# Performance work log

Hardware: AMD Instinct MI355X
Metric: run time of the kernel (lower is better)

The kernel has to match this reference:

```python
import jax, jax.numpy as jnp
import numpy as np

N_NODES = 50000
N_EDGES = 800000
OBS_DIM = 25
HID = 128
EMB = 64
EDGE_DIM = 8
HEADS = 4
N_LAYERS = 3
COMM_RANGE = 1500.0
LN_EPS = 1e-5


def layernorm(x, g, b):
    mu = jnp.mean(x, axis=-1, keepdims=True)
    var = jnp.mean((x - mu) ** 2, axis=-1, keepdims=True)
    return (x - mu) / jnp.sqrt(var + LN_EPS) * g + b


def setup_inputs() -> dict:
    key = jax.random.key(0)
    ks = iter(jax.random.split(key, 64))

    def w(shape, s=0.05):
        return (jax.random.normal(next(ks), shape, jnp.float32) * s).astype(jnp.float32)

    inp = {}
    inp["observations"] = jax.random.normal(next(ks), (N_NODES, OBS_DIM), jnp.float32)
    inp["positions"] = jax.random.uniform(next(ks), (N_NODES, 2), jnp.float32) * 1000.0
    inp["edge_index"] = jax.random.randint(next(ks), (2, N_EDGES), 0, N_NODES, jnp.int32)
    # node encoder (obs_encoder branch: Linear-LN-ReLU-Linear-ReLU)
    inp["enc_w1"] = w((OBS_DIM, HID)); inp["enc_b1"] = w((HID,), 0.01)
    inp["enc_ln_g"] = jnp.ones((HID,), jnp.float32); inp["enc_ln_b"] = jnp.zeros((HID,), jnp.float32)
    inp["enc_w2"] = w((HID, EMB)); inp["enc_b2"] = w((EMB,), 0.01)
    cat_dim = 2 * EMB + EDGE_DIM  # 136
    # per-layer GNN params, stacked over layers
    inp["msg_w1"] = w((N_LAYERS, cat_dim, HID)); inp["msg_b1"] = w((N_LAYERS, HID), 0.01)
    inp["msg_w2"] = w((N_LAYERS, HID, EMB)); inp["msg_b2"] = w((N_LAYERS, EMB), 0.01)
    inp["att_w1"] = w((N_LAYERS, cat_dim, HID)); inp["att_b1"] = w((N_LAYERS, HID), 0.01)
    inp["att_w2"] = w((N_LAYERS, HID, HEADS)); inp["att_b2"] = w((N_LAYERS, HEADS), 0.01)
    inp["upd_w1"] = w((N_LAYERS, 2 * EMB, HID)); inp["upd_b1"] = w((N_LAYERS, HID), 0.01)
    inp["upd_w2"] = w((N_LAYERS, HID, EMB)); inp["upd_b2"] = w((N_LAYERS, EMB), 0.01)
    inp["ln_g"] = jnp.ones((N_LAYERS, EMB), jnp.float32); inp["ln_b"] = jnp.zeros((N_LAYERS, EMB), jnp.float32)
    # output projection
    inp["out_w1"] = w((EMB, HID)); inp["out_b1"] = w((HID,), 0.01)
    inp["out_w2"] = w((HID, EMB)); inp["out_b2"] = w((EMB,), 0.01)
    return inp


def reference(observations, positions, edge_index,
              enc_w1, enc_b1, enc_ln_g, enc_ln_b, enc_w2, enc_b2,
              msg_w1, msg_b1, msg_w2, msg_b2,
              att_w1, att_b1, att_w2, att_b2,
              upd_w1, upd_b1, upd_w2, upd_b2,
              ln_g, ln_b,
              out_w1, out_b1, out_w2, out_b2):
    n = observations.shape[0]
    # --- node encoder (use_full_obs=True path) ---
    h = observations @ enc_w1 + enc_b1
    h = jax.nn.relu(layernorm(h, enc_ln_g, enc_ln_b))
    x = jax.nn.relu(h @ enc_w2 + enc_b2)  # [N, EMB]

    # --- edge features (build_graph math, edges given) ---
    src, dst = edge_index[0], edge_index[1]
    rel = positions[dst] - positions[src]                    # [E, 2]
    dist = jnp.linalg.norm(rel, axis=-1, keepdims=True)      # [E, 1]
    rel_n = rel / (dist + 1e-6)
    dist_n = dist / COMM_RANGE
    angle = jnp.arctan2(rel[:, 1], rel[:, 0])[:, None]
    edge_attr = jnp.concatenate(
        [dist_n, rel_n, jnp.cos(angle), jnp.sin(angle), dist_n ** 2,
         jnp.zeros((rel.shape[0], 2), x.dtype)], axis=-1)    # [E, 8]

    # --- GNN communication layers (PyG: x_i = target = dst, x_j = source = src,
    #     aggregate to dst; dropout inactive at inference) ---
    for l in range(N_LAYERS):
        cat = jnp.concatenate([x[dst], x[src], edge_attr], axis=-1)       # [E, 136]
        m = jax.nn.relu(cat @ msg_w1[l] + msg_b1[l]) @ msg_w2[l] + msg_b2[l]   # [E, EMB]
        a = jax.nn.relu(cat @ att_w1[l] + att_b1[l]) @ att_w2[l] + att_b2[l]   # [E, HEADS]
        wgt = jnp.mean(jax.nn.softmax(a, axis=-1), axis=-1, keepdims=True)     # [E, 1]
        aggr = jax.ops.segment_sum(m * wgt, dst, num_segments=n)               # [N, EMB]
        upd_in = jnp.concatenate([x, aggr], axis=-1)                            # [N, 2*EMB]
        upd = jax.nn.relu(upd_in @ upd_w1[l] + upd_b1[l]) @ upd_w2[l] + upd_b2[l]
        x = layernorm(x + upd, ln_g[l], ln_b[l])

    # --- output projection ---
    return jax.nn.relu(x @ out_w1 + out_b1) @ out_w2 + out_b2
```

## Files before the change

kernel.cpp:

```cpp
#include <hip/hip_runtime.h>
#include <hip/hip_bf16.h>

typedef unsigned short ushort_t;
typedef unsigned int uint_t;

constexpr int OBS  = 25;
constexpr int HID  = 128;
constexpr int EMB  = 64;
constexpr int CAT  = 136;
constexpr int NN   = 50000;

constexpr int TE      = 128;
constexpr int ETHR    = 512;
constexpr int K1PAD   = 148;
constexpr int K2PAD   = 140;
constexpr int K1STEPS = 9;
constexpr int K2STEPS = 8;

constexpr int TB = 128;

typedef __attribute__((ext_vector_type(8)))  short bf16x8;
typedef __attribute__((ext_vector_type(16))) float f32x16;
typedef __attribute__((ext_vector_type(4)))  uint_t uint4v;

__device__ __forceinline__ ushort_t f2bf(float f) {
    union { float f; uint_t u; } v; v.f = f;
    uint_t r = v.u + 0x7FFFu + ((v.u >> 16) & 1u);
    return (ushort_t)(r >> 16);
}

__device__ __forceinline__ bf16x8 ld8(const ushort_t* p) {
    uint2 lo = *reinterpret_cast<const uint2*>(p);
    uint2 hi = *reinterpret_cast<const uint2*>(p + 4);
    uint4 u = make_uint4(lo.x, lo.y, hi.x, hi.y);
// ... 50 lines not shown
    int e = blockIdx.x * 256 + threadIdx.x;
    if (e >= ne) return;
    int s = src[e], d = dst[e];
    float rx = pos[d * 2 + 0] - pos[s * 2 + 0];
    float ry = pos[d * 2 + 1] - pos[s * 2 + 1];
    float dist = sqrtf(rx * rx + ry * ry);
    float inv = 1.f / (dist + 1e-6f);
    float dn = dist * (1.f / 1500.f);
    uint_t ux = (uint_t)f2bf(dn) | ((uint_t)f2bf(rx * inv) << 16);
    uint_t uy = (uint_t)f2bf(ry * inv) | ((dist > 0.f ? 0u : 1u) << 16);
    int p = atomicAdd(&ofs[d], 1);
    uint4v ev = { ux, uy, (uint_t)s, (uint_t)d };
    eab4[p] = ev;
}

__global__ __launch_bounds__(256) void k_prep(
    const float* __restrict__ w1, const float* __restrict__ w2,
    ushort_t* __restrict__ w1t, ushort_t* __restrict__ w2t)
{
    int t = blockIdx.x * 256 + threadIdx.x;
    const int n1 = 3 * HID * K1PAD;
    if (t < n1) {
        int l = t / (HID * K1PAD), rem = t % (HID * K1PAD);
        int c = rem / K1PAD, k = rem % K1PAD;
        float v = (k < CAT) ? w1[(size_t)l * CAT * HID + (size_t)k * HID + c] : 0.f;
        w1t[t] = f2bf(v);
    }
    const int n2 = 3 * EMB * K2PAD;
    if (t < n2) {
        int l = t / (EMB * K2PAD), rem = t % (EMB * K2PAD);
        int c = rem / K2PAD, k = rem % K2PAD;
        float v = (k < HID) ? w2[(size_t)l * HID * EMB + (size_t)k * EMB + c] : 0.f;
        w2t[t] = f2bf(v);
    }
}

constexpr int EKP = 36;
__global__ __launch_bounds__(256, 1) void k_encoder_mfma(
    const float* __restrict__ obs,
    const float* __restrict__ w1, const float* __restrict__ b1,
    const float* __restrict__ lng, const float* __restrict__ lnb,
    const float* __restrict__ w2, const float* __restrict__ b2,
    float* __restrict__ x, ushort_t* __restrict__ xb, int n)
{
    __shared__ __align__(16) ushort_t s_OB[TB * EKP];
    __shared__ __align__(16) ushort_t s_B1[HID * EKP];
    __shared__ __align__(16) float    s_G[TB * 132];
    __shared__ __align__(16) ushort_t s_H[TB * K2PAD];
    __shared__ __align__(16) ushort_t s_W2[EMB * K2PAD];

    const int tid = threadIdx.x;
    const int lane = tid & 63, wid = tid >> 6;
    const int wr = wid >> 1, wc = wid & 1;
    const int l31 = lane & 31, lhi = lane >> 5;
    const int n0 = blockIdx.x * TB;

    for (int i = tid; i < TB * 32; i += 256) {
        int row = i >> 5, k = i & 31;
        int gn = n0 + row;
        float v = (gn < n && k < OBS) ? obs[(size_t)gn * OBS + k] : 0.f;
        s_OB[row * EKP + k] = f2bf(v);
    }
    for (int i = tid; i < 32 * HID; i += 256) {
        int k = i >> 7, c = i & 127;
        float v = (k < OBS) ? w1[k * HID + c] : 0.f;
        s_B1[c * EKP + k] = f2bf(v);
    }
    __syncthreads();

    f32x16 a00, a01, a10, a11;
    {
        float bv0 = b1[wc * 64 + l31], bv1 = b1[wc * 64 + 32 + l31];
#pragma unroll
        for (int i = 0; i < 16; ++i) { a00[i] = bv0; a01[i] = bv1; a10[i] = bv0; a11[i] = bv1; }
    }
    {
        const ushort_t* aR0 = s_OB + (wr * 64 + l31) * EKP;
        const ushort_t* aR1 = aR0 + 32 * EKP;
        const ushort_t* bR0 = s_B1 + (wc * 64 + l31) * EKP;
        const ushort_t* bR1 = bR0 + 32 * EKP;
        const int koff = lhi * 8;
#pragma unroll
        for (int s = 0; s < 2; ++s) {
            const int ke = s * 16 + koff;
            bf16x8 av0 = ld8(aR0 + ke), av1 = ld8(aR1 + ke);
            bf16x8 bv0 = ld8(bR0 + ke), bv1 = ld8(bR1 + ke);
            a00 = __builtin_amdgcn_mfma_f32_32x32x16_bf16(av0, bv0, a00, 0, 0, 0);
            a01 = __builtin_amdgcn_mfma_f32_32x32x16_bf16(av0, bv1, a01, 0, 0, 0);
            a10 = __builtin_amdgcn_mfma_f32_32x32x16_bf16(av1, bv0, a10, 0, 0, 0);
            a11 = __builtin_amdgcn_mfma_f32_32x32x16_bf16(av1, bv1, a11, 0, 0, 0);
        }
    }
#define WRITE_G(ACC, SUB, NC)                                                  \
    {                                                                          \
        const int col = wc * 64 + (NC) * 32 + l31;                             \
        _Pragma("unroll")                                                      \
        for (int r = 0; r < 16; ++r) {                                         \
            int row = wr * 64 + (SUB) * 32 + CROW(r, lhi);                     \
            s_G[row * 132 + col] = ACC[r];                                     \
        }                                                                      \
    }
    WRITE_G(a00, 0, 0) WRITE_G(a01, 0, 1) WRITE_G(a10, 1, 0) WRITE_G(a11, 1, 1)
#undef WRITE_G
    __syncthreads();

    for (int i = tid; i < HID * EMB; i += 256) {
        int k = i >> 6, c = i & 63;
        s_W2[c * K2PAD + k] = f2bf(w2[i]);
    }
    if (tid < TB) {
        float sum = 0.f, sum2 = 0.f;
        const float* gr = s_G + tid * 132;
#pragma unroll 8
        for (int q = 0; q < HID; ++q) { float v = gr[q]; sum += v; sum2 += v * v; }
        float mu = sum * (1.f / HID);
        float var = fmaxf(sum2 * (1.f / HID) - mu * mu, 0.f);
        float rs = 1.f / sqrtf(var + 1e-5f);
        ushort_t* hr = s_H + tid * K2PAD;
#pragma unroll 8
        for (int q = 0; q < HID; ++q) {
            float v = (gr[q] - mu) * rs * lng[q] + lnb[q];
            hr[q] = f2bf(fmaxf(v, 0.f));
        }
    }
    __syncthreads();

    f32x16 c0, c1;
    {
        float bv = b2[wc * 32 + l31];
#pragma unroll
        for (int i = 0; i < 16; ++i) { c0[i] = bv; c1[i] = bv; }
    }
    {
        const ushort_t* aR0 = s_H + (wr * 64 + l31) * K2PAD;
        const ushort_t* aR1 = aR0 + 32 * K2PAD;
        const ushort_t* bR = s_W2 + (wc * 32 + l31) * K2PAD;
        const int koff = lhi * 8;
#pragma unroll
        for (int s = 0; s < K2STEPS; ++s) {
            const int ke = s * 16 + koff;
            bf16x8 av0 = ld8(aR0 + ke), av1 = ld8(aR1 + ke);
            bf16x8 bv = ld8(bR + ke);
            c0 = __builtin_amdgcn_mfma_f32_32x32x16_bf16(av0, bv, c0, 0, 0, 0);
            c1 = __builtin_amdgcn_mfma_f32_32x32x16_bf16(av1, bv, c1, 0, 0, 0);
        }
    }
    {
        const int col = wc * 32 + l31;
#define STORE_X(CC, SUB)                                                       \
        {                                                                      \
            _Pragma("unroll")                                                  \
            for (int r = 0; r < 16; ++r) {                                     \
                int row = wr * 64 + (SUB) * 32 + CROW(r, lhi);                 \
                int gn = n0 + row;                                             \
                if (gn < n) {                                                  \
                    float v = fmaxf(CC[r], 0.f);                               \
                    x[(size_t)gn * EMB + col] = v;                             \
                    xb[(size_t)gn * EMB + col] = f2bf(v);                      \
                }                                                              \
            }                                                                  \
        }
        STORE_X(c0, 0) STORE_X(c1, 1)
#undef STORE_X
    }
}

__global__ __launch_bounds__(ETHR, 8) void k_edge_mfma(
    const ushort_t* __restrict__ xb,
    const uint4v* __restrict__ eab4,
    const ushort_t* __restrict__ w1t,
    const float* __restrict__ b1,
    const ushort_t* __restrict__ w2t,
    const float* __restrict__ b2,
    float* __restrict__ aggr, int ne)
{
    __shared__ __align__(16) ushort_t s_A[TE * K1PAD];
    __shared__ int s_dst[TE];
    ushort_t* s_H = s_A;
// ... 57 lines not shown
        const ushort_t* bR0 = w1t + (wc * 64 + l31) * K1PAD;
        const ushort_t* bR1 = bR0 + 32 * K1PAD;
        const int koff = lhi * 8;
#pragma unroll
        for (int s = 0; s < K1STEPS; ++s) {
            const int ke = s * 16 + koff;
            bf16x8 av = ld8(aR + ke);
            bf16x8 bv0 = ld8(bR0 + ke);
            bf16x8 bv1 = ld8(bR1 + ke);
            a0 = __builtin_amdgcn_mfma_f32_32x32x16_bf16(av, bv0, a0, 0, 0, 0);
            a1 = __builtin_amdgcn_mfma_f32_32x32x16_bf16(av, bv1, a1, 0, 0, 0);
        }
    }
    __syncthreads();

#define WRITE_H(ACC, NC)                                                       \
    {                                                                          \
        const int col = wc * 64 + (NC) * 32 + l31;                             \
        _Pragma("unroll")                                                      \
        for (int r = 0; r < 16; ++r) {                                         \
            int row = wr * 32 + CROW(r, lhi);                                  \
            s_H[row * K2PAD + col] = f2bf(fmaxf(ACC[r], 0.f));                 \
        }                                                                      \
    }
    WRITE_H(a0, 0) WRITE_H(a1, 1)
#undef WRITE_H
    __syncthreads();

    f32x16 c0;
    {
        float bv = b2[wc * 32 + l31];
#pragma unroll
        for (int i = 0; i < 16; ++i) c0[i] = bv;
    }
    {
        const ushort_t* aR = s_H + (wr * 32 + l31) * K2PAD;
        const ushort_t* bR = w2t + (wc * 32 + l31) * K2PAD;
        const int koff = lhi * 8;
#pragma unroll
        for (int s = 0; s < K2STEPS; ++s) {
            const int ke = s * 16 + koff;
// ... 20 lines not shown
        float acc = 0.f;
#pragma unroll 8
        for (int r = 0; r < 32; ++r) {
            int d = s_dst[base + r];
            float v = s_M[(base + r) * 68 + col];
            if (d != cur) {
                atomicAdd(aggr + (size_t)cur * EMB + col, acc);
                acc = 0.f; cur = d;
            }
            acc += v;
        }
        atomicAdd(aggr + (size_t)cur * EMB + col, acc);
    }
}

__global__ __launch_bounds__(256, 2) void k_update_mfma(
    float* __restrict__ x, ushort_t* __restrict__ xb,
    float* __restrict__ aggr,
    const float* __restrict__ w1, const float* __restrict__ b1,
    const float* __restrict__ w2, const float* __restrict__ b2,
    const float* __restrict__ g, const float* __restrict__ bb, int n)
{
    __shared__ __align__(16) ushort_t s_A[TB * K2PAD];
    __shared__ __align__(16) ushort_t s_B[TB * K2PAD];
    ushort_t* s_H  = s_A;
    ushort_t* s_W2 = s_B;
    float*    s_U  = reinterpret_cast<float*>(s_B);

    const int tid = threadIdx.x;
    const int lane = tid & 63, wid = tid >> 6;
    const int wr = wid >> 1, wc = wid & 1;
    const int l31 = lane & 31, lhi = lane >> 5;
    const int n0 = blockIdx.x * TB;

    {
        const int row = tid >> 1, h = tid & 1;
        const int gn = n0 + row;
        ushort_t* arow = s_A + row * K2PAD;
        if (h == 0) {
            uint2* dp = reinterpret_cast<uint2*>(arow);
            if (gn < n) {
                const uint2* sp = reinterpret_cast<const uint2*>(xb + (size_t)gn * EMB);
#pragma unroll
                for (int i = 0; i < 16; ++i) dp[i] = sp[i];
            } else {
                const uint2 z = make_uint2(0u, 0u);
#pragma unroll
                for (int i = 0; i < 16; ++i) dp[i] = z;
            }
        } else {
            if (gn < n) {
                float4* sp = reinterpret_cast<float4*>(aggr + (size_t)gn * EMB);
                const float4 z4 = make_float4(0.f, 0.f, 0.f, 0.f);
#pragma unroll
                for (int i = 0; i < 16; ++i) {
                    float4 v = sp[i];
                    sp[i] = z4;
                    ushort_t* qq = arow + EMB + i * 4;
                    qq[0] = f2bf(v.x); qq[1] = f2bf(v.y); qq[2] = f2bf(v.z); qq[3] = f2bf(v.w);
                }
            } else {
#pragma unroll
                for (int i = 0; i < 16; ++i) {
                    ushort_t* qq = arow + EMB + i * 4;
                    qq[0] = 0; qq[1] = 0; qq[2] = 0; qq[3] = 0;
                }
            }
        }
    }
    for (int i = tid; i < 128 * 128; i += 256) {
        int k = i >> 7, c = i & 127;
        s_B[c * K2PAD + k] = f2bf(w1[i]);
    }
    __syncthreads();

    f32x16 a00, a01, a10, a11;
    {
        float bv0 = b1[wc * 64 + l31], bv1 = b1[wc * 64 + 32 + l31];
#pragma unroll
        for (int i = 0; i < 16; ++i) { a00[i] = bv0; a01[i] = bv1; a10[i] = bv0; a11[i] = bv1; }
    }
    {
        const ushort_t* aR0 = s_A + (wr * 64 + l31) * K2PAD;
        const ushort_t* aR1 = aR0 + 32 * K2PAD;
        const ushort_t* bR0 = s_B + (wc * 64 + l31) * K2PAD;
        const ushort_t* bR1 = bR0 + 32 * K2PAD;
        const int koff = lhi * 8;
#pragma unroll
        for (int s = 0; s < K2STEPS; ++s) {
            const int ke = s * 16 + koff;
            bf16x8 av0 = ld8(aR0 + ke), av1 = ld8(aR1 + ke);
            bf16x8 bv0 = ld8(bR0 + ke), bv1 = ld8(bR1 + ke);
            a00 = __builtin_amdgcn_mfma_f32_32x32x16_bf16(av0, bv0, a00, 0, 0, 0);
            a01 = __builtin_amdgcn_mfma_f32_32x32x16_bf16(av0, bv1, a01, 0, 0, 0);
            a10 = __builtin_amdgcn_mfma_f32_32x32x16_bf16(av1, bv0, a10, 0, 0, 0);
            a11 = __builtin_amdgcn_mfma_f32_32x32x16_bf16(av1, bv1, a11, 0, 0, 0);
        }
    }
    __syncthreads();

#define WRITE_H(ACC, SUB, NC)                                                  \
    {                                                                          \
        const int col = wc * 64 + (NC) * 32 + l31;                             \
        _Pragma("unroll")                                                      \
        for (int r = 0; r < 16; ++r) {                                         \
            int row = wr * 64 + (SUB) * 32 + CROW(r, lhi);                     \
            s_H[row * K2PAD + col] = f2bf(fmaxf(ACC[r], 0.f));                 \
        }                                                                      \
    }
    WRITE_H(a00, 0, 0) WRITE_H(a01, 0, 1) WRITE_H(a10, 1, 0) WRITE_H(a11, 1, 1)
#undef WRITE_H
    for (int i = tid; i < HID * EMB; i += 256) {
        int k = i >> 6, c = i & 63;
        s_W2[c * K2PAD + k] = f2bf(w2[i]);
    }
    __syncthreads();

    f32x16 c0, c1;
    {
        float bv = b2[wc * 32 + l31];
#pragma unroll
        for (int i = 0; i < 16; ++i) { c0[i] = bv; c1[i] = bv; }
    }
    {
        const ushort_t* aR0 = s_H + (wr * 64 + l31) * K2PAD;
        const ushort_t* aR1 = aR0 + 32 * K2PAD;
        const ushort_t* bR = s_W2 + (wc * 32 + l31) * K2PAD;
        const int koff = lhi * 8;
#pragma unroll
        for (int s = 0; s < K2STEPS; ++s) {
            const int ke = s * 16 + koff;
            bf16x8 av0 = ld8(aR0 + ke), av1 = ld8(aR1 + ke);
            bf16x8 bv = ld8(bR + ke);
            c0 = __builtin_amdgcn_mfma_f32_32x32x16_bf16(av0, bv, c0, 0, 0, 0);
            c1 = __builtin_amdgcn_mfma_f32_32x32x16_bf16(av1, bv, c1, 0, 0, 0);
        }
    }
    __syncthreads();

    {
        const int col = wc * 32 + l31;
#pragma unroll
        for (int r = 0; r < 16; ++r) {
            int row = wr * 64 + CROW(r, lhi);
            s_U[row * 68 + col] = c0[r];
            s_U[(row + 32) * 68 + col] = c1[r];
        }
    }
    __syncthreads();

    if (tid < TB) {
        int gn = n0 + tid;
        if (gn < n) {
            const float* xr = x + (size_t)gn * EMB;
            float* ur = s_U + tid * 68;
            float sum = 0.f, sum2 = 0.f;
#pragma unroll 8
            for (int q = 0; q < EMB; ++q) {
                float v = xr[q] + ur[q];
                ur[q] = v;
                sum += v; sum2 += v * v;
            }
            float mu = sum * (1.f / EMB);
            float var = fmaxf(sum2 * (1.f / EMB) - mu * mu, 0.f);
            float rs = 1.f / sqrtf(var + 1e-5f);
            float* xo = x + (size_t)gn * EMB;
            ushort_t* xbo = xb + (size_t)gn * EMB;
#pragma unroll 8
            for (int q = 0; q < EMB; ++q) {
                float v = (ur[q] - mu) * rs * g[q] + bb[q];
                xo[q] = v;
                xbo[q] = f2bf(v);
            }
        }
    }
}

constexpr int OKP = 68;
__global__ __launch_bounds__(256, 2) void k_output_mfma(
    const ushort_t* __restrict__ xb,
    const float* __restrict__ w1, const float* __restrict__ b1,
    const float* __restrict__ w2, const float* __restrict__ b2,
    float* __restrict__ out, int n)
{
    __shared__ __align__(16) ushort_t s_A[TB * OKP];
    __shared__ __align__(16) ushort_t s_B[HID * OKP];
    __shared__ __align__(16) ushort_t s_H[TB * K2PAD];
    __shared__ __align__(16) ushort_t s_W2[EMB * K2PAD];

    const int tid = threadIdx.x;
    const int lane = tid & 63, wid = tid >> 6;
    const int wr = wid >> 1, wc = wid & 1;
    const int l31 = lane & 31, lhi = lane >> 5;
    const int n0 = blockIdx.x * TB;

    for (int i = tid; i < TB * 16; i += 256) {
        int row = i >> 4, q = i & 15;
        int gn = n0 + row;
        uint2 v = make_uint2(0u, 0u);
        if (gn < n) v = reinterpret_cast<const uint2*>(xb + (size_t)gn * EMB)[q];
        *reinterpret_cast<uint2*>(s_A + row * OKP + q * 4) = v;
    }
    for (int i = tid; i < EMB * HID; i += 256) {
        int k = i >> 7, c = i & 127;
        s_B[c * OKP + k] = f2bf(w1[i]);
    }
    for (int i = tid; i < HID * EMB; i += 256) {
        int k = i >> 6, c = i & 63;
        s_W2[c * K2PAD + k] = f2bf(w2[i]);
    }
    __syncthreads();

    f32x16 a00, a01, a10, a11;
    {
        float bv0 = b1[wc * 64 + l31], bv1 = b1[wc * 64 + 32 + l31];
#pragma unroll
        for (int i = 0; i < 16; ++i) { a00[i] = bv0; a01[i] = bv1; a10[i] = bv0; a11[i] = bv1; }
    }
    {
        const ushort_t* aR0 = s_A + (wr * 64 + l31) * OKP;
        const ushort_t* aR1 = aR0 + 32 * OKP;
        const ushort_t* bR0 = s_B + (wc * 64 + l31) * OKP;
        const ushort_t* bR1 = bR0 + 32 * OKP;
        const int koff = lhi * 8;
#pragma unroll
        for (int s = 0; s < 4; ++s) {
            const int ke = s * 16 + koff;
            bf16x8 av0 = ld8(aR0 + ke), av1 = ld8(aR1 + ke);
            bf16x8 bv0 = ld8(bR0 + ke), bv1 = ld8(bR1 + ke);
            a00 = __builtin_amdgcn_mfma_f32_32x32x16_bf16(av0, bv0, a00, 0, 0, 0);
            a01 = __builtin_amdgcn_mfma_f32_32x32x16_bf16(av0, bv1, a01, 0, 0, 0);
            a10 = __builtin_amdgcn_mfma_f32_32x32x16_bf16(av1, bv0, a10, 0, 0, 0);
            a11 = __builtin_amdgcn_mfma_f32_32x32x16_bf16(av1, bv1, a11, 0, 0, 0);
        }
    }
    __syncthreads();

#define WRITE_H(ACC, SUB, NC)                                                  \
    {                                                                          \
        const int col = wc * 64 + (NC) * 32 + l31;                             \
        _Pragma("unroll")                                                      \
        for (int r = 0; r < 16; ++r) {                                         \
            int row = wr * 64 + (SUB) * 32 + CROW(r, lhi);                     \
            s_H[row * K2PAD + col] = f2bf(fmaxf(ACC[r], 0.f));                 \
        }                                                                      \
    }
    WRITE_H(a00, 0, 0) WRITE_H(a01, 0, 1) WRITE_H(a10, 1, 0) WRITE_H(a11, 1, 1)
#undef WRITE_H
    __syncthreads();

    f32x16 c0, c1;
    {
        float bv = b2[wc * 32 + l31];
#pragma unroll
        for (int i = 0; i < 16; ++i) { c0[i] = bv; c1[i] = bv; }
    }
    {
        const ushort_t* aR0 = s_H + (wr * 64 + l31) * K2PAD;
        const ushort_t* aR1 = aR0 + 32 * K2PAD;
        const ushort_t* bR = s_W2 + (wc * 32 + l31) * K2PAD;
        const int koff = lhi * 8;
#pragma unroll
        for (int s = 0; s < K2STEPS; ++s) {
            const int ke = s * 16 + koff;
            bf16x8 av0 = ld8(aR0 + ke), av1 = ld8(aR1 + ke);
            bf16x8 bv = ld8(bR + ke);
            c0 = __builtin_amdgcn_mfma_f32_32x32x16_bf16(av0, bv, c0, 0, 0, 0);
            c1 = __builtin_amdgcn_mfma_f32_32x32x16_bf16(av1, bv, c1, 0, 0, 0);
        }
    }
    {
        const int col = wc * 32 + l31;
#pragma unroll
        for (int r = 0; r < 16; ++r) {
            int row0 = wr * 64 + CROW(r, lhi);
            int g0 = n0 + row0, g1 = g0 + 32;
            if (g0 < n) out[(size_t)g0 * EMB + col] = c0[r];
            if (g1 < n) out[(size_t)g1 * EMB + col] = c1[r];
        }
    }
}

extern "C" void kernel_launch(void* const* d_in, const int* in_sizes, int n_in,
                              void* d_out, int out_size, void* d_ws, size_t ws_size,
                              hipStream_t stream)
{
    const float* obs     = (const float*)d_in[0];
    const float* pos     = (const float*)d_in[1];
    const int*   eidx    = (const int*)d_in[2];
    const float* enc_w1  = (const float*)d_in[3];
    const float* enc_b1  = (const float*)d_in[4];
    const float* enc_lng = (const float*)d_in[5];
    const float* enc_lnb = (const float*)d_in[6];
// ... 12 lines not shown
    const float* out_w1  = (const float*)d_in[23];
    const float* out_b1  = (const float*)d_in[24];
    const float* out_w2  = (const float*)d_in[25];
    const float* out_b2  = (const float*)d_in[26];

    const int n  = in_sizes[0] / OBS;
    const int ne = in_sizes[2] / 2;
    const int* src = eidx;
    const int* dst = eidx + ne;

    char* ws = (char*)d_ws;
    float*    x     = (float*)ws;
    ushort_t* xbuf  = (ushort_t*)(ws + 12800000);
    uint4v*   eab4  = (uint4v*)(ws + 19200000);
    float*    aggr  = (float*)(ws + 32000000);
    ushort_t* w1t   = (ushort_t*)(ws + 44800000);
    ushort_t* w2t   = (ushort_t*)(ws + 44913664);
    int*      hist  = (int*)(ws + 44967424);
    int*      scan  = (int*)(ws + 45167424);
    int*      bsum  = (int*)(ws + 45367424);

    const int NB1 = (NN + 511) / 512;
    const int nb  = (n + TB - 1) / TB;

    hipMemsetAsync(hist, 0, NN * sizeof(int), stream);
    k_hist<<<(ne + 255) / 256, 256, 0, stream>>>(dst, hist, ne);
    k_scan1<<<NB1, 512, 0, stream>>>(hist, scan, bsum, NN);
    k_scan3<<<NB1, 512, 0, stream>>>(scan, bsum, NN);
    k_scatter_feat<<<(ne + 255) / 256, 256, 0, stream>>>(pos, src, dst, scan,
                                                         eab4, ne);

    k_prep<<<(3 * HID * K1PAD + 255) / 256, 256, 0, stream>>>(msg_w1, msg_w2, w1t, w2t);
    k_encoder_mfma<<<nb, 256, 0, stream>>>(obs, enc_w1, enc_b1, enc_lng, enc_lnb,
                                           enc_w2, enc_b2, x, xbuf, n);
    hipMemsetAsync(aggr, 0, (size_t)n * EMB * sizeof(float), stream);

    for (int l = 0; l < 3; ++l) {
        k_edge_mfma<<<ne / TE, ETHR, 0, stream>>>(
            xbuf, eab4,
            w1t + (size_t)l * HID * K1PAD, msg_b1 + (size_t)l * HID,
            w2t + (size_t)l * EMB * K2PAD, msg_b2 + (size_t)l * EMB,
            aggr, ne);
        k_update_mfma<<<nb, 256, 0, stream>>>(
            x, xbuf, aggr,
            upd_w1 + (size_t)l * 2 * EMB * HID, upd_b1 + (size_t)l * HID,
            upd_w2 + (size_t)l * HID * EMB, upd_b2 + (size_t)l * EMB,
            ln_g + (size_t)l * EMB, ln_b + (size_t)l * EMB, n);
    }
    k_output_mfma<<<nb, 256, 0, stream>>>(
        xbuf, out_w1, out_b1, out_w2, out_b2, (float*)d_out, n);
}
```

Before: 713.8 us.

## Pretranspose all weights once, shrink node tiles, fuse output projection into last update

Every weight matrix (update, encoder, output) is now converted to padded transposed bf16 in one prep kernel, so node kernels read MFMA B-operands straight from global memory instead of rebuilding them in shared memory per block. Node kernels use 64-row tiles with less LDS, allowing higher occupancy (launch bounds raised to 2 and 4 blocks per CU). The output MLP is fused into the final update kernel through a flag, which removes one launch and one pass over the node features. In exchange, B-operand reads now go through cache rather than LDS, and the extra prep work adds some overhead.

After: 678.3 us. -5.0%, faster.

```diff
diff --git a/kernel.cpp b/kernel.cpp
--- a/kernel.cpp
+++ b/kernel.cpp
@@ -17,7 +17,9 @@
 constexpr int K1STEPS = 9;
 constexpr int K2STEPS = 8;
 
-constexpr int TB = 128;
+constexpr int TBN = 64;
+constexpr int EKP = 36;
+constexpr int XKP = 68;
 
 typedef __attribute__((ext_vector_type(8)))  short bf16x8;
 typedef __attribute__((ext_vector_type(16))) float f32x16;
@@ -98,101 +100,118 @@
     eab4[p] = ev;
 }
 
-__global__ __launch_bounds__(256) void k_prep(
-    const float* __restrict__ w1, const float* __restrict__ w2,
-    ushort_t* __restrict__ w1t, ushort_t* __restrict__ w2t)
+__global__ __launch_bounds__(256) void k_prep_all(
+    const float* __restrict__ msg_w1, const float* __restrict__ msg_w2,
+    const float* __restrict__ upd_w1, const float* __restrict__ upd_w2,
+    const float* __restrict__ enc_w1, const float* __restrict__ enc_w2,
+    const float* __restrict__ out_w1, const float* __restrict__ out_w2,
+    ushort_t* __restrict__ mw1t, ushort_t* __restrict__ mw2t,
+    ushort_t* __restrict__ uw1t, ushort_t* __restrict__ uw2t,
+    ushort_t* __restrict__ ew1t, ushort_t* __restrict__ ew2t,
+    ushort_t* __restrict__ ow1t, ushort_t* __restrict__ ow2t)
 {
     int t = blockIdx.x * 256 + threadIdx.x;
-    const int n1 = 3 * HID * K1PAD;
-    if (t < n1) {
-        int l = t / (HID * K1PAD), rem = t % (HID * K1PAD);
-        int c = rem / K1PAD, k = rem % K1PAD;
-        float v = (k < CAT) ? w1[(size_t)l * CAT * HID + (size_t)k * HID + c] : 0.f;
-        w1t[t] = f2bf(v);
-    }
-    const int n2 = 3 * EMB * K2PAD;
-    if (t < n2) {
-        int l = t / (EMB * K2PAD), rem = t % (EMB * K2PAD);
-        int c = rem / K2PAD, k = rem % K2PAD;
-        float v = (k < HID) ? w2[(size_t)l * HID * EMB + (size_t)k * EMB + c] : 0.f;
-        w2t[t] = f2bf(v);
-    }
-}
-
-constexpr int EKP = 36;
-__global__ __launch_bounds__(256, 1) void k_encoder_mfma(
+    const int S0 = 3 * HID * K1PAD, S1 = 3 * EMB * K2PAD;
+    const int S2 = 3 * HID * K2PAD, S3 = 3 * EMB * K2PAD;
+    const int S4 = HID * EKP, S5 = EMB * K2PAD;
+    const int S6 = HID * XKP, S7 = EMB * K2PAD;
+    if (t < S0) {
+        int l = t / (HID * K1PAD), r = t % (HID * K1PAD), c = r / K1PAD, k = r % K1PAD;
+        mw1t[t] = f2bf(k < CAT ? msg_w1[(size_t)l * CAT * HID + (size_t)k * HID + c] : 0.f);
+        return;
+    } t -= S0;
+    if (t < S1) {
+        int l = t / (EMB * K2PAD), r = t % (EMB * K2PAD), c = r / K2PAD, k = r % K2PAD;
+        mw2t[t] = f2bf(k < HID ? msg_w2[(size_t)l * HID * EMB + (size_t)k * EMB + c] : 0.f);
+        return;
+    } t -= S1;
+    if (t < S2) {
+        int l = t / (HID * K2PAD), r = t % (HID * K2PAD), c = r / K2PAD, k = r % K2PAD;
+        uw1t[t] = f2bf(k < 2 * EMB ? upd_w1[(size_t)l * 2 * EMB * HID + (size_t)k * HID + c] : 0.f);
+        return;
+    } t -= S2;
+    if (t < S3) {
+        int l = t / (EMB * K2PAD), r = t % (EMB * K2PAD), c = r / K2PAD, k = r % K2PAD;
+        uw2t[t] = f2bf(k < HID ? upd_w2[(size_t)l * HID * EMB + (size_t)k * EMB + c] : 0.f);
+        return;
+    } t -= S3;
+    if (t < S4) {
+        int c = t / EKP, k = t % EKP;
+        ew1t[t] = f2bf(k < OBS ? enc_w1[(size_t)k * HID + c] : 0.f);
+        return;
+    } t -= S4;
+    if (t < S5) {
+        int c = t / K2PAD, k = t % K2PAD;
+        ew2t[t] = f2bf(k < HID ? enc_w2[(size_t)k * EMB + c] : 0.f);
+        return;
+    } t -= S5;
+    if (t < S6) {
+        int c = t / XKP, k = t % XKP;
+        ow1t[t] = f2bf(k < EMB ? out_w1[(size_t)k * HID + c] : 0.f);
+        return;
+    } t -= S6;
+    if (t < S7) {
+        int c = t / K2PAD, k = t % K2PAD;
+        ow2t[t] = f2bf(k < HID ? out_w2[(size_t)k * EMB + c] : 0.f);
+    }
+}
+
+__global__ __launch_bounds__(256, 2) void k_encoder_mfma(
     const float* __restrict__ obs,
-    const float* __restrict__ w1, const float* __restrict__ b1,
+    const ushort_t* __restrict__ w1t, const float* __restrict__ b1,
     const float* __restrict__ lng, const float* __restrict__ lnb,
-    const float* __restrict__ w2, const float* __restrict__ b2,
+    const ushort_t* __restrict__ w2t, const float* __restrict__ b2,
     float* __restrict__ x, ushort_t* __restrict__ xb, int n)
 {
-    __shared__ __align__(16) ushort_t s_OB[TB * EKP];
-    __shared__ __align__(16) ushort_t s_B1[HID * EKP];
-    __shared__ __align__(16) float    s_G[TB * 132];
-    __shared__ __align__(16) ushort_t s_H[TB * K2PAD];
-    __shared__ __align__(16) ushort_t s_W2[EMB * K2PAD];
+    __shared__ __align__(16) ushort_t s_OB[TBN * EKP];
+    __shared__ __align__(16) float    s_G[TBN * 132];
+    __shared__ __align__(16) ushort_t s_H[TBN * K2PAD];
 
     const int tid = threadIdx.x;
     const int lane = tid & 63, wid = tid >> 6;
-    const int wr = wid >> 1, wc = wid & 1;
+    const int wr = wid >> 1, wc2 = wid & 1;
+    const int wr2 = wid & 1, wc3 = wid >> 1;
     const int l31 = lane & 31, lhi = lane >> 5;
-    const int n0 = blockIdx.x * TB;
-
-    for (int i = tid; i < TB * 32; i += 256) {
+    const int n0 = blockIdx.x * TBN;
+
+    for (int i = tid; i < TBN * 32; i += 256) {
         int row = i >> 5, k = i & 31;
         int gn = n0 + row;
-        float v = (gn < n && k < OBS) ? obs[(size_t)gn * OBS + k] : 0.f;
-        s_OB[row * EKP + k] = f2bf(v);
-    }
-    for (int i = tid; i < 32 * HID; i += 256) {
-        int k = i >> 7, c = i & 127;
-        float v = (k < OBS) ? w1[k * HID + c] : 0.f;
-        s_B1[c * EKP + k] = f2bf(v);
-    }
-    __syncthreads();
-
-    f32x16 a00, a01, a10, a11;
-    {
-        float bv0 = b1[wc * 64 + l31], bv1 = b1[wc * 64 + 32 + l31];
-#pragma unroll
-        for (int i = 0; i < 16; ++i) { a00[i] = bv0; a01[i] = bv1; a10[i] = bv0; a11[i] = bv1; }
-    }
-    {
-        const ushort_t* aR0 = s_OB + (wr * 64 + l31) * EKP;
-        const ushort_t* aR1 = aR0 + 32 * EKP;
-        const ushort_t* bR0 = s_B1 + (wc * 64 + l31) * EKP;
+        s_OB[row * EKP + k] = f2bf((gn < n && k < OBS) ? obs[(size_t)gn * OBS + k] : 0.f);
+    }
+    __syncthreads();
+
+    f32x16 a0, a1;
+    {
+        float bv0 = b1[wc2 * 64 + l31], bv1 = b1[wc2 * 64 + 32 + l31];
+#pragma unroll
+        for (int i = 0; i < 16; ++i) { a0[i] = bv0; a1[i] = bv1; }
+    }
+    {
+        const ushort_t* aR = s_OB + (wr * 32 + l31) * EKP;
+        const ushort_t* bR0 = w1t + (wc2 * 64 + l31) * EKP;
         const ushort_t* bR1 = bR0 + 32 * EKP;
         const int koff = lhi * 8;
 #pragma unroll
         for (int s = 0; s < 2; ++s) {
             const int ke = s * 16 + koff;
-            bf16x8 av0 = ld8(aR0 + ke), av1 = ld8(aR1 + ke);
+            bf16x8 av = ld8(aR + ke);
             bf16x8 bv0 = ld8(bR0 + ke), bv1 = ld8(bR1 + ke);
-            a00 = __builtin_amdgcn_mfma_f32_32x32x16_bf16(av0, bv0, a00, 0, 0, 0);
-            a01 = __builtin_amdgcn_mfma_f32_32x32x16_bf16(av0, bv1, a01, 0, 0, 0);
-            a10 = __builtin_amdgcn_mfma_f32_32x32x16_bf16(av1, bv0, a10, 0, 0, 0);
-            a11 = __builtin_amdgcn_mfma_f32_32x32x16_bf16(av1, bv1, a11, 0, 0, 0);
-        }
-    }
-#define WRITE_G(ACC, SUB, NC)                                                  \
-    {                                                                          \
-        const int col = wc * 64 + (NC) * 32 + l31;                             \
-        _Pragma("unroll")                                                      \
-        for (int r = 0; r < 16; ++r) {                                         \
-            int row = wr * 64 + (SUB) * 32 + CROW(r, lhi);                     \
-            s_G[row * 132 + col] = ACC[r];                                     \
-        }                                                                      \
-    }
-    WRITE_G(a00, 0, 0) WRITE_G(a01, 0, 1) WRITE_G(a10, 1, 0) WRITE_G(a11, 1, 1)
-#undef WRITE_G
-    __syncthreads();
-
-    for (int i = tid; i < HID * EMB; i += 256) {
-        int k = i >> 6, c = i & 63;
-        s_W2[c * K2PAD + k] = f2bf(w2[i]);
-    }
-    if (tid < TB) {
+            a0 = __builtin_amdgcn_mfma_f32_32x32x16_bf16(av, bv0, a0, 0, 0, 0);
+            a1 = __builtin_amdgcn_mfma_f32_32x32x16_bf16(av, bv1, a1, 0, 0, 0);
+        }
+    }
+    {
+#pragma unroll
+        for (int r = 0; r < 16; ++r) {
+            int row = wr * 32 + CROW(r, lhi);
+            s_G[row * 132 + wc2 * 64 + l31] = a0[r];
+            s_G[row * 132 + wc2 * 64 + 32 + l31] = a1[r];
+        }
+    }
+    __syncthreads();
+
+    if (tid < TBN) {
         float sum = 0.f, sum2 = 0.f;
         const float* gr = s_G + tid * 132;
 #pragma unroll 8
@@ -209,43 +228,35 @@
     }
     __syncthreads();
 
-    f32x16 c0, c1;
-    {
-        float bv = b2[wc * 32 + l31];
-#pragma unroll
-        for (int i = 0; i < 16; ++i) { c0[i] = bv; c1[i] = bv; }
-    }
-    {
-        const ushort_t* aR0 = s_H + (wr * 64 + l31) * K2PAD;
-        const ushort_t* aR1 = aR0 + 32 * K2PAD;
-        const ushort_t* bR = s_W2 + (wc * 32 + l31) * K2PAD;
+    f32x16 c0;
+    {
+        float bv = b2[wc3 * 32 + l31];
+#pragma unroll
+        for (int i = 0; i < 16; ++i) c0[i] = bv;
+    }
+    {
+        const ushort_t* aR = s_H + (wr2 * 32 + l31) * K2PAD;
+        const ushort_t* bR = w2t + (wc3 * 32 + l31) * K2PAD;
         const int koff = lhi * 8;
 #pragma unroll
         for (int s = 0; s < K2STEPS; ++s) {
             const int ke = s * 16 + koff;
-            bf16x8 av0 = ld8(aR0 + ke), av1 = ld8(aR1 + ke);
+            bf16x8 av = ld8(aR + ke);
             bf16x8 bv = ld8(bR + ke);
-            c0 = __builtin_amdgcn_mfma_f32_32x32x16_bf16(av0, bv, c0, 0, 0, 0);
-            c1 = __builtin_amdgcn_mfma_f32_32x32x16_bf16(av1, bv, c1, 0, 0, 0);
-        }
-    }
-    {
-        const int col = wc * 32 + l31;
-#define STORE_X(CC, SUB)                                                       \
-        {                                                                      \
-            _Pragma("unroll")                                                  \
-            for (int r = 0; r < 16; ++r) {                                     \
-                int row = wr * 64 + (SUB) * 32 + CROW(r, lhi);                 \
-                int gn = n0 + row;                                             \
-                if (gn < n) {                                                  \
-                    float v = fmaxf(CC[r], 0.f);                               \
-                    x[(size_t)gn * EMB + col] = v;                             \
-                    xb[(size_t)gn * EMB + col] = f2bf(v);                      \
-                }                                                              \
-            }                                                                  \
-        }
-        STORE_X(c0, 0) STORE_X(c1, 1)
-#undef STORE_X
+            c0 = __builtin_amdgcn_mfma_f32_32x32x16_bf16(av, bv, c0, 0, 0, 0);
+        }
+    }
+    {
+        const int col = wc3 * 32 + l31;
+#pragma unroll
+        for (int r = 0; r < 16; ++r) {
+            int g = n0 + wr2 * 32 + CROW(r, lhi);
+            if (g < n) {
+                float v = fmaxf(c0[r], 0.f);
+                x[(size_t)g * EMB + col] = v;
+                xb[(size_t)g * EMB + col] = f2bf(v);
+            }
+        }
     }
 }
 
@@ -333,7 +344,7 @@
     }
     __syncthreads();
 
-#define WRITE_H(ACC, NC)                                                       \
+#define WRITE_HE(ACC, NC)                                                      \
     {                                                                          \
         const int col = wc * 64 + (NC) * 32 + l31;                             \
         _Pragma("unroll")                                                      \
@@ -342,8 +353,8 @@
             s_H[row * K2PAD + col] = f2bf(fmaxf(ACC[r], 0.f));                 \
         }                                                                      \
     }
-    WRITE_H(a0, 0) WRITE_H(a1, 1)
-#undef WRITE_H
+    WRITE_HE(a0, 0) WRITE_HE(a1, 1)
+#undef WRITE_HE
     __syncthreads();
 
     f32x16 c0;
@@ -394,269 +405,230 @@
     }
 }
 
-__global__ __launch_bounds__(256, 2) void k_update_mfma(
+__global__ __launch_bounds__(256, 4) void k_update_mfma(
     float* __restrict__ x, ushort_t* __restrict__ xb,
     float* __restrict__ aggr,
-    const float* __restrict__ w1, const float* __restrict__ b1,
-    const float* __restrict__ w2, const float* __restrict__ b2,
-    const float* __restrict__ g, const float* __restrict__ bb, int n)
-{
-    __shared__ __align__(16) ushort_t s_A[TB * K2PAD];
-    __shared__ __align__(16) ushort_t s_B[TB * K2PAD];
-    ushort_t* s_H  = s_A;
-    ushort_t* s_W2 = s_B;
-    float*    s_U  = reinterpret_cast<float*>(s_B);
+    const ushort_t* __restrict__ w1t, const float* __restrict__ b1,
+    const ushort_t* __restrict__ w2t, const float* __restrict__ b2,
+    const float* __restrict__ g, const float* __restrict__ bb,
+    const ushort_t* __restrict__ ow1t, const float* __restrict__ ob1,
+    const ushort_t* __restrict__ ow2t, const float* __restrict__ ob2,
+    float* __restrict__ out, int fuse, int n)
+{
+    __shared__ __align__(16) ushort_t s_big[TBN * K2PAD];
+    __shared__ __align__(16) ushort_t s_Xn[TBN * XKP];
+    ushort_t* s_A = s_big;
+    ushort_t* s_H = s_big;
+    float*    s_U = reinterpret_cast<float*>(s_big);
 
     const int tid = threadIdx.x;
     const int lane = tid & 63, wid = tid >> 6;
-    const int wr = wid >> 1, wc = wid & 1;
+    const int wr = wid >> 1, wc2 = wid & 1;
+    const int wr2 = wid & 1, wc3 = wid >> 1;
     const int l31 = lane & 31, lhi = lane >> 5;
-    const int n0 = blockIdx.x * TB;
-
-    {
-        const int row = tid >> 1, h = tid & 1;
+    const int n0 = blockIdx.x * TBN;
+
+    {
+        const int row = tid >> 2, h = tid & 3;
         const int gn = n0 + row;
         ushort_t* arow = s_A + row * K2PAD;
-        if (h == 0) {
-            uint2* dp = reinterpret_cast<uint2*>(arow);
+        if (h < 2) {
+            uint2* dp = reinterpret_cast<uint2*>(arow) + h * 8;
             if (gn < n) {
-                const uint2* sp = reinterpret_cast<const uint2*>(xb + (size_t)gn * EMB);
-#pragma unroll
-                for (int i = 0; i < 16; ++i) dp[i] = sp[i];
+                const uint2* sp = reinterpret_cast<const uint2*>(xb + (size_t)gn * EMB) + h * 8;
+#pragma unroll
+                for (int i = 0; i < 8; ++i) dp[i] = sp[i];
             } else {
                 const uint2 z = make_uint2(0u, 0u);
 #pragma unroll
-                for (int i = 0; i < 16; ++i) dp[i] = z;
+                for (int i = 0; i < 8; ++i) dp[i] = z;
             }
         } else {
+            const int hh = h - 2;
+            uint_t* dp32 = reinterpret_cast<uint_t*>(arow + EMB + hh * 32);
             if (gn < n) {
-                float4* sp = reinterpret_cast<float4*>(aggr + (size_t)gn * EMB);
+                float4* sp = reinterpret_cast<float4*>(aggr + (size_t)gn * EMB + hh * 32);
                 const float4 z4 = make_float4(0.f, 0.f, 0.f, 0.f);
 #pragma unroll
-                for (int i = 0; i < 16; ++i) {
+                for (int i = 0; i < 8; ++i) {
                     float4 v = sp[i];
                     sp[i] = z4;
-                    ushort_t* qq = arow + EMB + i * 4;
-                    qq[0] = f2bf(v.x); qq[1] = f2bf(v.y); qq[2] = f2bf(v.z); qq[3] = f2bf(v.w);
+                    dp32[2 * i]     = (uint_t)f2bf(v.x) | ((uint_t)f2bf(v.y) << 16);
+                    dp32[2 * i + 1] = (uint_t)f2bf(v.z) | ((uint_t)f2bf(v.w) << 16);
                 }
             } else {
 #pragma unroll
-                for (int i = 0; i < 16; ++i) {
-                    ushort_t* qq = arow + EMB + i * 4;
-                    qq[0] = 0; qq[1] = 0; qq[2] = 0; qq[3] = 0;
+                for (int i = 0; i < 16; ++i) dp32[i] = 0u;
+            }
+        }
+    }
+    __syncthreads();
+
+    f32x16 a0, a1;
+    {
+        float bv0 = b1[wc2 * 64 + l31], bv1 = b1[wc2 * 64 + 32 + l31];
+#pragma unroll
+        for (int i = 0; i < 16; ++i) { a0[i] = bv0; a1[i] = bv1; }
+    }
+    {
+        const ushort_t* aR = s_A + (wr * 32 + l31) * K2PAD;
+        const ushort_t* bR0 = w1t + (wc2 * 64 + l31) * K2PAD;
+        const ushort_t* bR1 = bR0 + 32 * K2PAD;
+        const int koff = lhi * 8;
+#pragma unroll
+        for (int s = 0; s < K2STEPS; ++s) {
+            const int ke = s * 16 + koff;
+            bf16x8 av = ld8(aR + ke);
+            bf16x8 bv0 = ld8(bR0 + ke), bv1 = ld8(bR1 + ke);
+            a0 = __builtin_amdgcn_mfma_f32_32x32x16_bf16(av, bv0, a0, 0, 0, 0);
+            a1 = __builtin_amdgcn_mfma_f32_32x32x16_bf16(av, bv1, a1, 0, 0, 0);
+        }
+    }
+    __syncthreads();
+
+#define WRITE_HU(ACC, NC)                                                      \
+    {                                                                          \
+        const int col = wc2 * 64 + (NC) * 32 + l31;                            \
+        _Pragma("unroll")                                                      \
+        for (int r = 0; r < 16; ++r) {                                         \
+            int row = wr * 32 + CROW(r, lhi);                                  \
+            s_H[row * K2PAD + col] = f2bf(fmaxf(ACC[r], 0.f));                 \
+        }                                                                      \
+    }
+    WRITE_HU(a0, 0) WRITE_HU(a1, 1)
+    __syncthreads();
+
+    f32x16 c0;
+    {
+        float bv = b2[wc3 * 32 + l31];
+#pragma unroll
+        for (int i = 0; i < 16; ++i) c0[i] = bv;
+    }
+    {
+        const ushort_t* aR = s_H + (wr2 * 32 + l31) * K2PAD;
+        const ushort_t* bR = w2t + (wc3 * 32 + l31) * K2PAD;
+        const int koff = lhi * 8;
+#pragma unroll
+        for (int s = 0; s < K2STEPS; ++s) {
+            const int ke = s * 16 + koff;
+            bf16x8 av = ld8(aR + ke);
+            bf16x8 bv = ld8(bR + ke);
+            c0 = __builtin_amdgcn_mfma_f32_32x32x16_bf16(av, bv, c0, 0, 0, 0);
+        }
+    }
+    __syncthreads();
+
+    {
+        const int col = wc3 * 32 + l31;
+#pragma unroll
+        for (int r = 0; r < 16; ++r) {
+            int row = wr2 * 32 + CROW(r, lhi);
+            s_U[row * 68 + col] = c0[r];
+        }
+    }
+    __syncthreads();
+
+    if (!fuse) {
+        if (tid < TBN) {
+            int gn = n0 + tid;
+            if (gn < n) {
+                const float* xr = x + (size_t)gn * EMB;
+                float* ur = s_U + tid * 68;
+                float sum = 0.f, sum2 = 0.f;
+#pragma unroll 8
+                for (int q = 0; q < EMB; ++q) {
+                    float v = xr[q] + ur[q];
+                    ur[q] = v;
+                    sum += v; sum2 += v * v;
+                }
+                float mu = sum * (1.f / EMB);
+                float var = fmaxf(sum2 * (1.f / EMB) - mu * mu, 0.f);
+                float rs = 1.f / sqrtf(var + 1e-5f);
+                float* xo = x + (size_t)gn * EMB;
+                ushort_t* xbo = xb + (size_t)gn * EMB;
+#pragma unroll 8
+                for (int q = 0; q < EMB; ++q) {
+                    float v = (ur[q] - mu) * rs * g[q] + bb[q];
+                    xo[q] = v;
+                    xbo[q] = f2bf(v);
                 }
             }
         }
-    }
-    for (int i = tid; i < 128 * 128; i += 256) {
-        int k = i >> 7, c = i & 127;
-        s_B[c * K2PAD + k] = f2bf(w1[i]);
-    }
-    __syncthreads();
-
-    f32x16 a00, a01, a10, a11;
-    {
-        float bv0 = b1[wc * 64 + l31], bv1 = b1[wc * 64 + 32 + l31];
-#pragma unroll
-        for (int i = 0; i < 16; ++i) { a00[i] = bv0; a01[i] = bv1; a10[i] = bv0; a11[i] = bv1; }
-    }
-    {
-        const ushort_t* aR0 = s_A + (wr * 64 + l31) * K2PAD;
-        const ushort_t* aR1 = aR0 + 32 * K2PAD;
-        const ushort_t* bR0 = s_B + (wc * 64 + l31) * K2PAD;
-        const ushort_t* bR1 = bR0 + 32 * K2PAD;
-        const int koff = lhi * 8;
-#pragma unroll
-        for (int s = 0; s < K2STEPS; ++s) {
-            const int ke = s * 16 + koff;
-            bf16x8 av0 = ld8(aR0 + ke), av1 = ld8(aR1 + ke);
-            bf16x8 bv0 = ld8(bR0 + ke), bv1 = ld8(bR1 + ke);
-            a00 = __builtin_amdgcn_mfma_f32_32x32x16_bf16(av0, bv0, a00, 0, 0, 0);
-            a01 = __builtin_amdgcn_mfma_f32_32x32x16_bf16(av0, bv1, a01, 0, 0, 0);
-            a10 = __builtin_amdgcn_mfma_f32_32x32x16_bf16(av1, bv0, a10, 0, 0, 0);
-            a11 = __builtin_amdgcn_mfma_f32_32x32x16_bf16(av1, bv1, a11, 0, 0, 0);
-        }
-    }
-    __syncthreads();
-
-#define WRITE_H(ACC, SUB, NC)                                                  \
-    {                                                                          \
-        const int col = wc * 64 + (NC) * 32 + l31;                             \
-        _Pragma("unroll")                                                      \
-        for (int r = 0; r < 16; ++r) {                                         \
-            int row = wr * 64 + (SUB) * 32 + CROW(r, lhi);                     \
-            s_H[row * K2PAD + col] = f2bf(fmaxf(ACC[r], 0.f));                 \
-        }                                                                      \
-    }
-    WRITE_H(a00, 0, 0) WRITE_H(a01, 0, 1) WRITE_H(a10, 1, 0) WRITE_H(a11, 1, 1)
-#undef WRITE_H
-    for (int i = tid; i < HID * EMB; i += 256) {
-        int k = i >> 6, c = i & 63;
-        s_W2[c * K2PAD + k] = f2bf(w2[i]);
-    }
-    __syncthreads();
-
-    f32x16 c0, c1;
-    {
-        float bv = b2[wc * 32 + l31];
-#pragma unroll
-        for (int i = 0; i < 16; ++i) { c0[i] = bv; c1[i] = bv; }
-    }
-    {
-        const ushort_t* aR0 = s_H + (wr * 64 + l31) * K2PAD;
-        const ushort_t* aR1 = aR0 + 32 * K2PAD;
-        const ushort_t* bR = s_W2 + (wc * 32 + l31) * K2PAD;
-        const int koff = lhi * 8;
-#pragma unroll
-        for (int s = 0; s < K2STEPS; ++s) {
-            const int ke = s * 16 + koff;
-            bf16x8 av0 = ld8(aR0 + ke), av1 = ld8(aR1 + ke);
-            bf16x8 bv = ld8(bR + ke);
-            c0 = __builtin_amdgcn_mfma_f32_32x32x16_bf16(av0, bv, c0, 0, 0, 0);
-            c1 = __builtin_amdgcn_mfma_f32_32x32x16_bf16(av1, bv, c1, 0, 0, 0);
-        }
-    }
-    __syncthreads();
-
-    {
-        const int col = wc * 32 + l31;
-#pragma unroll
-        for (int r = 0; r < 16; ++r) {
-            int row = wr * 64 + CROW(r, lhi);
-            s_U[row * 68 + col] = c0[r];
-            s_U[(row + 32) * 68 + col] = c1[r];
-        }
-    }
-    __syncthreads();
-
-    if (tid < TB) {
+        return;
+    }
+
+    if (tid < TBN) {
         int gn = n0 + tid;
         if (gn < n) {
             const float* xr = x + (size_t)gn * EMB;
-            float* ur = s_U + tid * 68;
+            const float* ur = s_U + tid * 68;
             float sum = 0.f, sum2 = 0.f;
 #pragma unroll 8
             for (int q = 0; q < EMB; ++q) {
                 float v = xr[q] + ur[q];
-                ur[q] = v;
                 sum += v; sum2 += v * v;
             }
             float mu = sum * (1.f / EMB);
             float var = fmaxf(sum2 * (1.f / EMB) - mu * mu, 0.f);
             float rs = 1.f / sqrtf(var + 1e-5f);
-            float* xo = x + (size_t)gn * EMB;
-            ushort_t* xbo = xb + (size_t)gn * EMB;
+            ushort_t* xnr = s_Xn + tid * XKP;
 #pragma unroll 8
             for (int q = 0; q < EMB; ++q) {
-                float v = (ur[q] - mu) * rs * g[q] + bb[q];
-                xo[q] = v;
-                xbo[q] = f2bf(v);
+                float v = (xr[q] + ur[q] - mu) * rs * g[q] + bb[q];
+                xnr[q] = f2bf(v);
             }
         }
     }
-}
-
-constexpr int OKP = 68;
-__global__ __launch_bounds__(256, 2) void k_output_mfma(
-    const ushort_t* __restrict__ xb,
-    const float* __restrict__ w1, const float* __restrict__ b1,
-    const float* __restrict__ w2, const float* __restrict__ b2,
-    float* __restrict__ out, int n)
-{
-    __shared__ __align__(16) ushort_t s_A[TB * OKP];
-    __shared__ __align__(16) ushort_t s_B[HID * OKP];
-    __shared__ __align__(16) ushort_t s_H[TB * K2PAD];
-    __shared__ __align__(16) ushort_t s_W2[EMB * K2PAD];
-
-    const int tid = threadIdx.x;
-    const int lane = tid & 63, wid = tid >> 6;
-    const int wr = wid >> 1, wc = wid & 1;
-    const int l31 = lane & 31, lhi = lane >> 5;
-    const int n0 = blockIdx.x * TB;
-
-    for (int i = tid; i < TB * 16; i += 256) {
-        int row = i >> 4, q = i & 15;
-        int gn = n0 + row;
-        uint2 v = make_uint2(0u, 0u);
-        if (gn < n) v = reinterpret_cast<const uint2*>(xb + (size_t)gn * EMB)[q];
-        *reinterpret_cast<uint2*>(s_A + row * OKP + q * 4) = v;
-    }
-    for (int i = tid; i < EMB * HID; i += 256) {
-        int k = i >> 7, c = i & 127;
-        s_B[c * OKP + k] = f2bf(w1[i]);
-    }
-    for (int i = tid; i < HID * EMB; i += 256) {
-        int k = i >> 6, c = i & 63;
-        s_W2[c * K2PAD + k] = f2bf(w2[i]);
-    }
-    __syncthreads();
-
-    f32x16 a00, a01, a10, a11;
-    {
-        float bv0 = b1[wc * 64 + l31], bv1 = b1[wc * 64 + 32 + l31];
-#pragma unroll
-        for (int i = 0; i < 16; ++i) { a00[i] = bv0; a01[i] = bv1; a10[i] = bv0; a11[i] = bv1; }
-    }
-    {
-        const ushort_t* aR0 = s_A + (wr * 64 + l31) * OKP;
-        const ushort_t* aR1 = aR0 + 32 * OKP;
-        const ushort_t* bR0 = s_B + (wc * 64 + l31) * OKP;
-        const ushort_t* bR1 = bR0 + 32 * OKP;
+    __syncthreads();
+
+    f32x16 o0, o1;
+    {
+        float bv0 = ob1[wc2 * 64 + l31], bv1 = ob1[wc2 * 64 + 32 + l31];
+#pragma unroll
+        for (int i = 0; i < 16; ++i) { o0[i] = bv0; o1[i] = bv1; }
+    }
+    {
+        const ushort_t* aR = s_Xn + (wr * 32 + l31) * XKP;
+        const ushort_t* bR0 = ow1t + (wc2 * 64 + l31) * XKP;
+        const ushort_t* bR1 = bR0 + 32 * XKP;
         const int koff = lhi * 8;
 #pragma unroll
         for (int s = 0; s < 4; ++s) {
             const int ke = s * 16 + koff;
-            bf16x8 av0 = ld8(aR0 + ke), av1 = ld8(aR1 + ke);
+            bf16x8 av = ld8(aR + ke);
             bf16x8 bv0 = ld8(bR0 + ke), bv1 = ld8(bR1 + ke);
-            a00 = __builtin_amdgcn_mfma_f32_32x32x16_bf16(av0, bv0, a00, 0, 0, 0);
-            a01 = __builtin_amdgcn_mfma_f32_32x32x16_bf16(av0, bv1, a01, 0, 0, 0);
-            a10 = __builtin_amdgcn_mfma_f32_32x32x16_bf16(av1, bv0, a10, 0, 0, 0);
-            a11 = __builtin_amdgcn_mfma_f32_32x32x16_bf16(av1, bv1, a11, 0, 0, 0);
-        }
-    }
-    __syncthreads();
-
-#define WRITE_H(ACC, SUB, NC)                                                  \
-    {                                                                          \
-        const int col = wc * 64 + (NC) * 32 + l31;                             \
-        _Pragma("unroll")                                                      \
-        for (int r = 0; r < 16; ++r) {                                         \
-            int row = wr * 64 + (SUB) * 32 + CROW(r, lhi);                     \
-            s_H[row * K2PAD + col] = f2bf(fmaxf(ACC[r], 0.f));                 \
-        }                                                                      \
-    }
-    WRITE_H(a00, 0, 0) WRITE_H(a01, 0, 1) WRITE_H(a10, 1, 0) WRITE_H(a11, 1, 1)
-#undef WRITE_H
-    __syncthreads();
-
-    f32x16 c0, c1;
-    {
-        float bv = b2[wc * 32 + l31];
-#pragma unroll
-        for (int i = 0; i < 16; ++i) { c0[i] = bv; c1[i] = bv; }
-    }
-    {
-        const ushort_t* aR0 = s_H + (wr * 64 + l31) * K2PAD;
-        const ushort_t* aR1 = aR0 + 32 * K2PAD;
-        const ushort_t* bR = s_W2 + (wc * 32 + l31) * K2PAD;
+            o0 = __builtin_amdgcn_mfma_f32_32x32x16_bf16(av, bv0, o0, 0, 0, 0);
+            o1 = __builtin_amdgcn_mfma_f32_32x32x16_bf16(av, bv1, o1, 0, 0, 0);
+        }
+    }
+    WRITE_HU(o0, 0) WRITE_HU(o1, 1)
+#undef WRITE_HU
+    __syncthreads();
+
+    f32x16 q0;
+    {
+        float bv = ob2[wc3 * 32 + l31];
+#pragma unroll
+        for (int i = 0; i < 16; ++i) q0[i] = bv;
+    }
+    {
+        const ushort_t* aR = s_H + (wr2 * 32 + l31) * K2PAD;
+        const ushort_t* bR = ow2t + (wc3 * 32 + l31) * K2PAD;
         const int koff = lhi * 8;
 #pragma unroll
         for (int s = 0; s < K2STEPS; ++s) {
             const int ke = s * 16 + koff;
-            bf16x8 av0 = ld8(aR0 + ke), av1 = ld8(aR1 + ke);
+            bf16x8 av = ld8(aR + ke);
             bf16x8 bv = ld8(bR + ke);
-            c0 = __builtin_amdgcn_mfma_f32_32x32x16_bf16(av0, bv, c0, 0, 0, 0);
-            c1 = __builtin_amdgcn_mfma_f32_32x32x16_bf16(av1, bv, c1, 0, 0, 0);
-        }
-    }
-    {
-        const int col = wc * 32 + l31;
+            q0 = __builtin_amdgcn_mfma_f32_32x32x16_bf16(av, bv, q0, 0, 0, 0);
+        }
+    }
+    {
+        const int col = wc3 * 32 + l31;
 #pragma unroll
         for (int r = 0; r < 16; ++r) {
-            int row0 = wr * 64 + CROW(r, lhi);
-            int g0 = n0 + row0, g1 = g0 + 32;
-            if (g0 < n) out[(size_t)g0 * EMB + col] = c0[r];
-            if (g1 < n) out[(size_t)g1 * EMB + col] = c1[r];
+            int grow = n0 + wr2 * 32 + CROW(r, lhi);
+            if (grow < n) out[(size_t)grow * EMB + col] = q0[r];
         }
     }
 }
@@ -699,14 +671,23 @@
     ushort_t* xbuf  = (ushort_t*)(ws + 12800000);
     uint4v*   eab4  = (uint4v*)(ws + 19200000);
     float*    aggr  = (float*)(ws + 32000000);
-    ushort_t* w1t   = (ushort_t*)(ws + 44800000);
-    ushort_t* w2t   = (ushort_t*)(ws + 44913664);
-    int*      hist  = (int*)(ws + 44967424);
-    int*      scan  = (int*)(ws + 45167424);
-    int*      bsum  = (int*)(ws + 45367424);
+    ushort_t* mw1t  = (ushort_t*)(ws + 44800000);
+    ushort_t* mw2t  = (ushort_t*)(ws + 44913664);
+    ushort_t* uw1t  = (ushort_t*)(ws + 44967424);
+    ushort_t* uw2t  = (ushort_t*)(ws + 45074944);
+    ushort_t* ew1t  = (ushort_t*)(ws + 45128704);
+    ushort_t* ew2t  = (ushort_t*)(ws + 45137920);
+    ushort_t* ow1t  = (ushort_t*)(ws + 45155840);
+    ushort_t* ow2t  = (ushort_t*)(ws + 45173248);
+    int*      hist  = (int*)(ws + 45191168);
+    int*      scan  = (int*)(ws + 45391168);
+    int*      bsum  = (int*)(ws + 45591168);
 
     const int NB1 = (NN + 511) / 512;
-    const int nb  = (n + TB - 1) / TB;
+    const int nbN = (n + TBN - 1) / TBN;
+    const int PREP_TOTAL = 3 * HID * K1PAD + 3 * EMB * K2PAD + 3 * HID * K2PAD
+                         + 3 * EMB * K2PAD + HID * EKP + EMB * K2PAD
+                         + HID * XKP + EMB * K2PAD;
 
     hipMemsetAsync(hist, 0, NN * sizeof(int), stream);
     k_hist<<<(ne + 255) / 256, 256, 0, stream>>>(dst, hist, ne);
@@ -715,23 +696,25 @@
     k_scatter_feat<<<(ne + 255) / 256, 256, 0, stream>>>(pos, src, dst, scan,
                                                          eab4, ne);
 
-    k_prep<<<(3 * HID * K1PAD + 255) / 256, 256, 0, stream>>>(msg_w1, msg_w2, w1t, w2t);
-    k_encoder_mfma<<<nb, 256, 0, stream>>>(obs, enc_w1, enc_b1, enc_lng, enc_lnb,
-                                           enc_w2, enc_b2, x, xbuf, n);
+    k_prep_all<<<(PREP_TOTAL + 255) / 256, 256, 0, stream>>>(
+        msg_w1, msg_w2, upd_w1, upd_w2, enc_w1, enc_w2, out_w1, out_w2,
+        mw1t, mw2t, uw1t, uw2t, ew1t, ew2t, ow1t, ow2t);
+    k_encoder_mfma<<<nbN, 256, 0, stream>>>(obs, ew1t, enc_b1, enc_lng, enc_lnb,
+                                            ew2t, enc_b2, x, xbuf, n);
     hipMemsetAsync(aggr, 0, (size_t)n * EMB * sizeof(float), stream);
 
     for (int l = 0; l < 3; ++l) {
         k_edge_mfma<<<ne / TE, ETHR, 0, stream>>>(
             xbuf, eab4,
-            w1t + (size_t)l * HID * K1PAD, msg_b1 + (size_t)l * HID,
-            w2t + (size_t)l * EMB * K2PAD, msg_b2 + (size_t)l * EMB,
+            mw1t + (size_t)l * HID * K1PAD, msg_b1 + (size_t)l * HID,
+            mw2t + (size_t)l * EMB * K2PAD, msg_b2 + (size_t)l * EMB,
             aggr, ne);
-        k_update_mfma<<<nb, 256, 0, stream>>>(
+        k_update_mfma<<<nbN, 256, 0, stream>>>(
             x, xbuf, aggr,
-            upd_w1 + (size_t)l * 2 * EMB * HID, upd_b1 + (size_t)l * HID,
-            upd_w2 + (size_t)l * HID * EMB, upd_b2 + (size_t)l * EMB,
-            ln_g + (size_t)l * EMB, ln_b + (size_t)l * EMB, n);
-    }
-    k_output_mfma<<<nb, 256, 0, stream>>>(
-        xbuf, out_w1, out_b1, out_w2, out_b2, (float*)d_out, n);
-}
+            uw1t + (size_t)l * HID * K2PAD, upd_b1 + (size_t)l * HID,
+            uw2t + (size_t)l * EMB * K2PAD, upd_b2 + (size_t)l * EMB,
+            ln_g + (size_t)l * EMB, ln_b + (size_t)l * EMB,
+            ow1t, out_b1, ow2t, out_b2,
+            (float*)d_out, (l == 2) ? 1 : 0, n);
+    }
+}
```
